# Kernel tuning notes

Hardware: AMD Instinct MI355X
Metric: run time of the kernel (lower is better)

## Reference

```python
import jax, jax.numpy as jnp
import numpy as np

N_NODES = 100000
IN_FEATURES = 128
OUT_FEATURES = 128
N_EDGES = 3200000


def setup_inputs() -> dict:
    key = jax.random.key(0)
    k1, k2, k3, k4, k5 = jax.random.split(key, 5)
    node_features = jax.random.normal(k1, (N_NODES, IN_FEATURES), dtype=jnp.float32)
    edge_index = jax.random.randint(k2, (2, N_EDGES), 0, N_NODES, dtype=jnp.int64)
    edge_values = jax.random.uniform(k3, (N_EDGES,), dtype=jnp.float32)
    # Linear layer params (PyTorch nn.Linear: y = x @ W.T + b)
    bound = 1.0 / np.sqrt(IN_FEATURES)
    W = jax.random.uniform(k4, (OUT_FEATURES, IN_FEATURES), minval=-bound, maxval=bound, dtype=jnp.float32)
    b = jax.random.uniform(k5, (OUT_FEATURES,), minval=-bound, maxval=bound, dtype=jnp.float32)
    return {"node_features": node_features, "edge_index": edge_index,
            "edge_values": edge_values, "W": W, "b": b}


def reference(node_features, edge_index, edge_values, W, b):
    n_nodes = node_features.shape[0]
    row, col = edge_index[0], edge_index[1]
    # zero diagonal entries, then square edge values
    vals = jnp.where(row != col, edge_values, jnp.zeros_like(edge_values)) ** 2
    # linear transform: [N, F_out]
    wx = node_features @ W.T + b
    # SpMM: temp[i] = sum_e vals[e] * wx[col[e]] for row[e] == i
    messages = vals[:, None] * wx[col]          # [E, F_out] gather + scale
    temp = jax.ops.segment_sum(messages, row, num_segments=n_nodes)  # scatter-add
    # Hadamard product
    return wx * temp
```

## Files before the change

kernel.cpp:

```cpp
#include <hip/hip_runtime.h>
#include <hip/hip_bf16.h>

#define F 128
#define RB 196
#define NB_MAX 511
#define BIN_CAP 16
#define NBLK_BIN 512
#define NXS 16

typedef __attribute__((ext_vector_type(8))) short bf16x8;
typedef __attribute__((ext_vector_type(4))) float f32x4;

static __device__ __forceinline__ short f2bf(float f) {
    __hip_bfloat16 h = __float2bfloat16(f);
    return __builtin_bit_cast(short, h);
}

__global__ __launch_bounds__(256) void gemm_mfma_kernel(
    const float* __restrict__ X, const float* __restrict__ W,
    const float* __restrict__ bias, float* __restrict__ wxf,
    __hip_bfloat16* __restrict__ wxh, int nrows)
{
    __shared__ short xs[128][136];
    __shared__ short wt[128][136];
    __shared__ float bsh[128];

    int t = threadIdx.x;
    long row0 = (long)blockIdx.x * 128;

    {
        int r = t >> 1, h = t & 1;
        const float4* src = reinterpret_cast<const float4*>(W + r * F + h * 64);
#pragma unroll
        for (int i = 0; i < 16; ++i) {
            float4 v = src[i];
            short4 s;
            s.x = f2bf(v.x); s.y = f2bf(v.y); s.z = f2bf(v.z); s.w = f2bf(v.w);
            *reinterpret_cast<short4*>(&wt[r][h * 64 + i * 4]) = s;
        }
        if (t < 128) bsh[t] = bias[t];
    }
    {
        int r = t >> 1, h = t & 1;
        long gr = row0 + r; if (gr > nrows - 1) gr = nrows - 1;
        const float4* src = reinterpret_cast<const float4*>(X + gr * F + h * 64);
#pragma unroll
        for (int i = 0; i < 16; ++i) {
            float4 v = src[i];
            short4 s;
            s.x = f2bf(v.x); s.y = f2bf(v.y); s.z = f2bf(v.z); s.w = f2bf(v.w);
            *reinterpret_cast<short4*>(&xs[r][h * 64 + i * 4]) = s;
        }
    }
    __syncthreads();

    int wave = t >> 6, lane = t & 63;
    int l15 = lane & 15, lg = lane >> 4;
    int mrow = wave * 32;

    float bj[8];
#pragma unroll
    for (int nf = 0; nf < 8; ++nf) bj[nf] = bsh[nf * 16 + l15];

    f32x4 acc[2][8] = {};

#pragma unroll
    for (int ks = 0; ks < 4; ++ks) {
        bf16x8 a0 = *reinterpret_cast<const bf16x8*>(&xs[mrow + l15][ks * 32 + lg * 8]);
        bf16x8 a1 = *reinterpret_cast<const bf16x8*>(&xs[mrow + 16 + l15][ks * 32 + lg * 8]);
#pragma unroll
        for (int nf = 0; nf < 8; ++nf) {
            bf16x8 bfr = *reinterpret_cast<const bf16x8*>(&wt[nf * 16 + l15][ks * 32 + lg * 8]);
            acc[0][nf] = __builtin_amdgcn_mfma_f32_16x16x32_bf16(a0, bfr, acc[0][nf], 0, 0, 0);
            acc[1][nf] = __builtin_amdgcn_mfma_f32_16x16x32_bf16(a1, bfr, acc[1][nf], 0, 0, 0);
        }
    }

#pragma unroll
    for (int mf = 0; mf < 2; ++mf) {
#pragma unroll
        for (int i = 0; i < 4; ++i) {
            long grow = row0 + mrow + mf * 16 + lg * 4 + i;
            if (grow < nrows) {
#pragma unroll
                for (int nf = 0; nf < 8; ++nf) {
                    float v = acc[mf][nf][i] + bj[nf];
                    int col = nf * 16 + l15;
                    wxf[grow * F + col] = v;
                    wxh[grow * F + col] = __float2bfloat16(v);
                }
            }
        }
    }
}

__global__ __launch_bounds__(256) void bin_edges_kernel(
    const int* __restrict__ rowi, const int* __restrict__ coli,
    const float* __restrict__ ev, int* __restrict__ cur2,
    int2* __restrict__ arena1, int E, int NB, int CAPX)
{
    __shared__ int2 bins[NB_MAX][BIN_CAP];
    __shared__ int  cnt[NB_MAX];
    __shared__ int  flushed[NB_MAX];

    int t = threadIdx.x;
    int x = blockIdx.x & (NXS - 1);
    for (int i = t; i < NB; i += 256) { cnt[i] = 0; flushed[i] = 0; }
    __syncthreads();

    long per   = ((long)E + NBLK_BIN - 1) / NBLK_BIN;
    long start = (long)blockIdx.x * per;
    long endE  = start + per; if (endE > E) endE = E;

    int r = 0, c = 0; float v = 0.f;
    {
        long i0 = start + t;
        if (i0 < endE) { r = rowi[i0]; c = coli[i0]; v = ev[i0]; }
    }

    for (long base = start; base < endE; base += 256) {
        if (base + t < endE) {
            float v2 = (r != c) ? v * v : 0.0f;
            int b  = r / RB;
            int rl = r - b * RB;
            int pos = atomicAdd(&cnt[b], 1);
            bins[b][pos & (BIN_CAP - 1)] = make_int2((rl << 17) | c, __float_as_int(v2));
        }
        int rn = 0, cn = 0; float vn = 0.f;
        {
            long i2 = base + 256 + t;
            if (i2 < endE) { rn = rowi[i2]; cn = coli[i2]; vn = ev[i2]; }
        }
        __syncthreads();
        for (int bb = t; bb < NB; bb += 256) {
            while (cnt[bb] - flushed[bb] >= 8) {
                int gpos = atomicAdd(&cur2[x * NB + bb], 8);
                if (gpos + 8 <= CAPX) {
                    const int2* src = &bins[bb][flushed[bb] & (BIN_CAP - 1)];
                    int2* dst = &arena1[((size_t)x * NB + bb) * CAPX + gpos];
                    const int4* s4 = (const int4*)src;
                    int4* d4 = (int4*)dst;
                    d4[0] = s4[0]; d4[1] = s4[1]; d4[2] = s4[2]; d4[3] = s4[3];
                }
                flushed[bb] += 8;
            }
        }
        __syncthreads();
        r = rn; c = cn; v = vn;
    }
    for (int bb = t; bb < NB; bb += 256) {
        int rem = cnt[bb] - flushed[bb];
        if (rem > 0) {
            int gpos = atomicAdd(&cur2[x * NB + bb], rem);
            if (gpos + rem <= CAPX) {
                int2* dst = &arena1[((size_t)x * NB + bb) * CAPX + gpos];
                for (int k = 0; k < rem; ++k)
                    dst[k] = bins[bb][(flushed[bb] + k) & (BIN_CAP - 1)];
            }
        }
    }
}

__global__ __launch_bounds__(256) void sort_bucket_kernel(
    const int* __restrict__ cur2, const int2* __restrict__ arena1,
    int2* __restrict__ arena2, int2* __restrict__ rowoff,
    int nrows, int NB, int CAPX, int CAP)
{
    __shared__ int rcnt[RB];
    __shared__ int rcur[RB];
    __shared__ int sscan[256];

    int b = blockIdx.x;
    int t = threadIdx.x;
    int2* dst = arena2 + (size_t)b * CAP;

    for (int i = t; i < RB; i += 256) rcnt[i] = 0;
    __syncthreads();

    for (int x = 0; x < NXS; ++x) {
        int n_x = cur2[x * NB + b]; if (n_x > CAPX) n_x = CAPX;
        const int2* seg = arena1 + ((size_t)x * NB + b) * CAPX;
        for (int i = t; i < n_x; i += 256)
            atomicAdd(&rcnt[seg[i].x >> 17], 1);
    }
    __syncthreads();

    int v = (t < RB) ? rcnt[t] : 0;
    sscan[t] = v;
    __syncthreads();
#pragma unroll
    for (int d = 1; d < 256; d <<= 1) {
        int u = (t >= d) ? sscan[t - d] : 0;
        __syncthreads();
        sscan[t] += u;
        __syncthreads();
    }
    if (t < RB) {
        int start = sscan[t] - v;
        rcur[t] = start;
        int grow = b * RB + t;
        if (grow < nrows)
            rowoff[grow] = make_int2(b * CAP + start, b * CAP + start + v);
    }
    __syncthreads();

    for (int x = 0; x < NXS; ++x) {
        int n_x = cur2[x * NB + b]; if (n_x > CAPX) n_x = CAPX;
        const int2* seg = arena1 + ((size_t)x * NB + b) * CAPX;
        for (int i = t; i < n_x; i += 256) {
            int2 rec = seg[i];
            int pos = atomicAdd(&rcur[rec.x >> 17], 1);
            if (pos < CAP) dst[pos] = rec;
        }
    }
}

__global__ __launch_bounds__(256) void agg_row_kernel(
    const int2* __restrict__ rowoff, const int2* __restrict__ arena2,
    const unsigned int* __restrict__ wxh32, float* __restrict__ outwx,
    int nrows)
{
    int wid  = (blockIdx.x * 256 + threadIdx.x) >> 6;
    int lane = threadIdx.x & 63;
    if (wid >= nrows) return;

    int2 se   = rowoff[wid];
    int start = __builtin_amdgcn_readfirstlane(se.x);
    int end   = __builtin_amdgcn_readfirstlane(se.y);

    float accx = 0.f, accy = 0.f;
    int e = start;
    for (; e + 3 < end; e += 4) {
        int2 r0 = arena2[e];
        int2 r1 = arena2[e + 1];
        int2 r2 = arena2[e + 2];
        int2 r3 = arena2[e + 3];
        unsigned int g0 = wxh32[(size_t)(r0.x & 0x1FFFF) * 64 + lane];
        unsigned int g1 = wxh32[(size_t)(r1.x & 0x1FFFF) * 64 + lane];
        unsigned int g2 = wxh32[(size_t)(r2.x & 0x1FFFF) * 64 + lane];
        unsigned int g3 = wxh32[(size_t)(r3.x & 0x1FFFF) * 64 + lane];
        float v0 = __int_as_float(r0.y), v1 = __int_as_float(r1.y);
        float v2 = __int_as_float(r2.y), v3 = __int_as_float(r3.y);
        accx = fmaf(v0, __uint_as_float(g0 << 16), accx);
        accy = fmaf(v0, __uint_as_float(g0 & 0xFFFF0000u), accy);
        accx = fmaf(v1, __uint_as_float(g1 << 16), accx);
        accy = fmaf(v1, __uint_as_float(g1 & 0xFFFF0000u), accy);
        accx = fmaf(v2, __uint_as_float(g2 << 16), accx);
        accy = fmaf(v2, __uint_as_float(g2 & 0xFFFF0000u), accy);
        accx = fmaf(v3, __uint_as_float(g3 << 16), accx);
        accy = fmaf(v3, __uint_as_float(g3 & 0xFFFF0000u), accy);
    }
    for (; e < end; ++e) {
        int2 r0 = arena2[e];
        unsigned int g0 = wxh32[(size_t)(r0.x & 0x1FFFF) * 64 + lane];
        float v0 = __int_as_float(r0.y);
        accx = fmaf(v0, __uint_as_float(g0 << 16), accx);
        accy = fmaf(v0, __uint_as_float(g0 & 0xFFFF0000u), accy);
    }

    float2 wr = *reinterpret_cast<const float2*>(outwx + (size_t)wid * F + lane * 2);
    float2 o;
    o.x = wr.x * accx;
    o.y = wr.y * accy;
    *reinterpret_cast<float2*>(outwx + (size_t)wid * F + lane * 2) = o;
}

__global__ __launch_bounds__(256) void edge_scatter_kernel(
    const int* __restrict__ rowi, const int* __restrict__ coli,
    const float* __restrict__ ev, const float* __restrict__ wx,
    float* __restrict__ temp, int E)
{
    int tid = blockIdx.x * 256 + threadIdx.x;
    int e   = tid >> 5;
    if (e >= E) return;
    int lane = tid & 31;
    int r = rowi[e];
    int c = coli[e];
    if (r == c) return;
    float v = ev[e];
    v = v * v;
    const float4 wv = *reinterpret_cast<const float4*>(wx + (size_t)c * F + lane * 4);
    float* tp = temp + (size_t)r * F + lane * 4;
    atomicAdd(tp + 0, v * wv.x);
    atomicAdd(tp + 1, v * wv.y);
    atomicAdd(tp + 2, v * wv.z);
    atomicAdd(tp + 3, v * wv.w);
}

__global__ __launch_bounds__(256) void finalize_kernel(
    float* __restrict__ out, const float* __restrict__ temp, int n4)
{
    int i = blockIdx.x * 256 + threadIdx.x;
    if (i >= n4) return;
    float4 o  = reinterpret_cast<float4*>(out)[i];
    float4 tv = reinterpret_cast<const float4*>(temp)[i];
    o.x *= tv.x; o.y *= tv.y; o.z *= tv.z; o.w *= tv.w;
    reinterpret_cast<float4*>(out)[i] = o;
}

__global__ void Interaction_GraphConvolution_55963423867450_kernel() {}

extern "C" void kernel_launch(void* const* d_in, const int* in_sizes, int n_in,
                              void* d_out, int out_size, void* d_ws, size_t ws_size,
                              hipStream_t stream)
{
    const float* X  = (const float*)d_in[0];
    const int*   ei = (const int*)d_in[1];
    const float* ev = (const float*)d_in[2];
    const float* W  = (const float*)d_in[3];
    const float* b  = (const float*)d_in[4];
    float* out = (float*)d_out;

    int nrows = in_sizes[0] / F;
    int E     = in_sizes[2];
    const int* rowi = ei;
    const int* coli = ei + E;

    int gblocks = (int)((nrows + 127) / 128);

    int NB = (nrows + RB - 1) / RB;
    if (NB <= NB_MAX) {
        long avg = (long)E / NB;
        int CAP  = (int)(((avg * 9) / 8 + 192 + 7) & ~7L);
        int CAPX = (int)(((avg / NXS) * 5 / 4 + 64 + 7) & ~7L);

        char* p = (char*)d_ws;
        __hip_bfloat16* wxh = (__hip_bfloat16*)p;
        p += (size_t)nrows * F * sizeof(__hip_bfloat16);
        int* cur2 = (int*)p;
        p += (size_t)NXS * NB * sizeof(int);
        p = (char*)(((uintptr_t)p + 63) & ~(uintptr_t)63);
        int2* rowoff = (int2*)p;
        p += (size_t)nrows * sizeof(int2);
        int2* arena1 = (int2*)p;
        p += (size_t)NXS * NB * CAPX * sizeof(int2);
        int2* arena2 = (int2*)p;
        p += (size_t)NB * CAP * sizeof(int2);
        size_t need = (size_t)(p - (char*)d_ws);

        if (ws_size >= need) {
            hipMemsetAsync(cur2, 0, (size_t)NXS * NB * sizeof(int), stream);
            gemm_mfma_kernel<<<gblocks, 256, 0, stream>>>(X, W, b, out, wxh, nrows);
            bin_edges_kernel<<<NBLK_BIN, 256, 0, stream>>>(rowi, coli, ev, cur2,
                                                           arena1, E, NB, CAPX);
            sort_bucket_kernel<<<NB, 256, 0, stream>>>(cur2, arena1, arena2,
                                                       rowoff, nrows, NB, CAPX, CAP);
            int ablocks = (int)(((long)nrows * 64 + 255) / 256);
            agg_row_kernel<<<ablocks, 256, 0, stream>>>(rowoff, arena2,
                                                        (const unsigned int*)wxh,
                                                        out, nrows);
            return;
        }
    }

    float* temp = (float*)d_ws;
    hipMemsetAsync(temp, 0, (size_t)nrows * F * sizeof(float), stream);
    __hip_bfloat16* wxh_dummy = (__hip_bfloat16*)((char*)d_ws + (size_t)nrows * F * sizeof(float));
    gemm_mfma_kernel<<<(int)((nrows + 127) / 128), 256, 0, stream>>>(X, W, b, out, wxh_dummy, nrows);
    long ethreads = (long)E * 32;
    int  eblocks32 = (int)((ethreads + 255) / 256);
    edge_scatter_kernel<<<eblocks32, 256, 0, stream>>>(rowi, coli, ev, out, temp, E);
    int n4 = nrows * F / 4;
    finalize_kernel<<<(n4 + 255) / 256, 256, 0, stream>>>(out, temp, n4);
}
```

Measured before the change: 224.6 us.

## Pack edge records into 32-bit bf16-value/col words and sort by column group

```diff
diff --git a/kernel.cpp b/kernel.cpp
--- a/kernel.cpp
+++ b/kernel.cpp
@@ -7,10 +7,16 @@
 #define BIN_CAP 16
 #define NBLK_BIN 512
 #define NXS 16
+#define NCG 16
+#define KEYS (RB * NCG)
 
 typedef __attribute__((ext_vector_type(8))) short bf16x8;
 typedef __attribute__((ext_vector_type(4))) float f32x4;
 
+static __device__ __forceinline__ unsigned short f2bfbits(float f) {
+    __hip_bfloat16 h = __float2bfloat16(f);
+    return __builtin_bit_cast(unsigned short, h);
+}
 static __device__ __forceinline__ short f2bf(float f) {
     __hip_bfloat16 h = __float2bfloat16(f);
     return __builtin_bit_cast(short, h);
@@ -163,30 +169,35 @@
 
 __global__ __launch_bounds__(256) void sort_bucket_kernel(
     const int* __restrict__ cur2, const int2* __restrict__ arena1,
-    int2* __restrict__ arena2, int2* __restrict__ rowoff,
+    unsigned int* __restrict__ arena2, int2* __restrict__ rowoff,
     int nrows, int NB, int CAPX, int CAP)
 {
-    __shared__ int rcnt[RB];
-    __shared__ int rcur[RB];
+    __shared__ int koff[KEYS];
     __shared__ int sscan[256];
 
     int b = blockIdx.x;
     int t = threadIdx.x;
-    int2* dst = arena2 + (size_t)b * CAP;
-
-    for (int i = t; i < RB; i += 256) rcnt[i] = 0;
+    unsigned int* dst = arena2 + (size_t)b * CAP;
+
+    for (int i = t; i < KEYS; i += 256) koff[i] = 0;
     __syncthreads();
 
     for (int x = 0; x < NXS; ++x) {
         int n_x = cur2[x * NB + b]; if (n_x > CAPX) n_x = CAPX;
         const int2* seg = arena1 + ((size_t)x * NB + b) * CAPX;
-        for (int i = t; i < n_x; i += 256)
-            atomicAdd(&rcnt[seg[i].x >> 17], 1);
-    }
-    __syncthreads();
-
-    int v = (t < RB) ? rcnt[t] : 0;
-    sscan[t] = v;
+        for (int i = t; i < n_x; i += 256) {
+            int rx = seg[i].x;
+            int key = (rx >> 17) * NCG + ((rx & 0x1FFFF) >> 13);
+            atomicAdd(&koff[key], 1);
+        }
+    }
+    __syncthreads();
+
+    const int PER = (KEYS + 255) / 256;
+    int lo = t * PER, hi = lo + PER; if (hi > KEYS) hi = KEYS; if (lo > KEYS) lo = KEYS;
+    int s = 0;
+    for (int i = lo; i < hi; ++i) s += koff[i];
+    sscan[t] = s;
     __syncthreads();
 #pragma unroll
     for (int d = 1; d < 256; d <<= 1) {
@@ -195,12 +206,22 @@
         sscan[t] += u;
         __syncthreads();
     }
+    int total = sscan[255];
+    int run = (t == 0) ? 0 : sscan[t - 1];
+    for (int i = lo; i < hi; ++i) {
+        int c0 = koff[i];
+        koff[i] = run;
+        run += c0;
+    }
+    __syncthreads();
+
     if (t < RB) {
-        int start = sscan[t] - v;
-        rcur[t] = start;
         int grow = b * RB + t;
-        if (grow < nrows)
-            rowoff[grow] = make_int2(b * CAP + start, b * CAP + start + v);
+        if (grow < nrows) {
+            int start = koff[t * NCG];
+            int end   = (t == RB - 1) ? total : koff[(t + 1) * NCG];
+            rowoff[grow] = make_int2(b * CAP + start, b * CAP + end);
+        }
     }
     __syncthreads();
 
@@ -209,14 +230,18 @@
         const int2* seg = arena1 + ((size_t)x * NB + b) * CAPX;
         for (int i = t; i < n_x; i += 256) {
             int2 rec = seg[i];
-            int pos = atomicAdd(&rcur[rec.x >> 17], 1);
-            if (pos < CAP) dst[pos] = rec;
+            int c = rec.x & 0x1FFFF;
+            int key = (rec.x >> 17) * NCG + (c >> 13);
+            int pos = atomicAdd(&koff[key], 1);
+            unsigned int pk = ((unsigned int)f2bfbits(__int_as_float(rec.y)) << 17)
+                              | (unsigned int)c;
+            if (pos < CAP) dst[pos] = pk;
         }
     }
 }
 
 __global__ __launch_bounds__(256) void agg_row_kernel(
-    const int2* __restrict__ rowoff, const int2* __restrict__ arena2,
+    const int2* __restrict__ rowoff, const unsigned int* __restrict__ arena2,
     const unsigned int* __restrict__ wxh32, float* __restrict__ outwx,
     int nrows)
 {
@@ -231,16 +256,18 @@
     float accx = 0.f, accy = 0.f;
     int e = start;
     for (; e + 3 < end; e += 4) {
-        int2 r0 = arena2[e];
-        int2 r1 = arena2[e + 1];
-        int2 r2 = arena2[e + 2];
-        int2 r3 = arena2[e + 3];
-        unsigned int g0 = wxh32[(size_t)(r0.x & 0x1FFFF) * 64 + lane];
-        unsigned int g1 = wxh32[(size_t)(r1.x & 0x1FFFF) * 64 + lane];
-        unsigned int g2 = wxh32[(size_t)(r2.x & 0x1FFFF) * 64 + lane];
-        unsigned int g3 = wxh32[(size_t)(r3.x & 0x1FFFF) * 64 + lane];
-        float v0 = __int_as_float(r0.y), v1 = __int_as_float(r1.y);
-        float v2 = __int_as_float(r2.y), v3 = __int_as_float(r3.y);
+        unsigned int p0 = arena2[e];
+        unsigned int p1 = arena2[e + 1];
+        unsigned int p2 = arena2[e + 2];
+        unsigned int p3 = arena2[e + 3];
+        unsigned int g0 = wxh32[(size_t)(p0 & 0x1FFFF) * 64 + lane];
+        unsigned int g1 = wxh32[(size_t)(p1 & 0x1FFFF) * 64 + lane];
+        unsigned int g2 = wxh32[(size_t)(p2 & 0x1FFFF) * 64 + lane];
+        unsigned int g3 = wxh32[(size_t)(p3 & 0x1FFFF) * 64 + lane];
+        float v0 = __uint_as_float((p0 >> 17) << 16);
+        float v1 = __uint_as_float((p1 >> 17) << 16);
+        float v2 = __uint_as_float((p2 >> 17) << 16);
+        float v3 = __uint_as_float((p3 >> 17) << 16);
         accx = fmaf(v0, __uint_as_float(g0 << 16), accx);
         accy = fmaf(v0, __uint_as_float(g0 & 0xFFFF0000u), accy);
         accx = fmaf(v1, __uint_as_float(g1 << 16), accx);
@@ -251,9 +278,9 @@
         accy = fmaf(v3, __uint_as_float(g3 & 0xFFFF0000u), accy);
     }
     for (; e < end; ++e) {
-        int2 r0 = arena2[e];
-        unsigned int g0 = wxh32[(size_t)(r0.x & 0x1FFFF) * 64 + lane];
-        float v0 = __int_as_float(r0.y);
+        unsigned int p0 = arena2[e];
+        unsigned int g0 = wxh32[(size_t)(p0 & 0x1FFFF) * 64 + lane];
+        float v0 = __uint_as_float((p0 >> 17) << 16);
         accx = fmaf(v0, __uint_as_float(g0 << 16), accx);
         accy = fmaf(v0, __uint_as_float(g0 & 0xFFFF0000u), accy);
     }
@@ -319,7 +346,7 @@
     int gblocks = (int)((nrows + 127) / 128);
 
     int NB = (nrows + RB - 1) / RB;
-    if (NB <= NB_MAX) {
+    if (NB <= NB_MAX && nrows < (1 << 17)) {
         long avg = (long)E / NB;
         int CAP  = (int)(((avg * 9) / 8 + 192 + 7) & ~7L);
         int CAPX = (int)(((avg / NXS) * 5 / 4 + 64 + 7) & ~7L);
@@ -334,8 +361,8 @@
         p += (size_t)nrows * sizeof(int2);
         int2* arena1 = (int2*)p;
         p += (size_t)NXS * NB * CAPX * sizeof(int2);
-        int2* arena2 = (int2*)p;
-        p += (size_t)NB * CAP * sizeof(int2);
+        unsigned int* arena2 = (unsigned int*)p;
+        p += (size_t)NB * CAP * sizeof(unsigned int);
         size_t need = (size_t)(p - (char*)d_ws);
 
         if (ws_size >= need) {
```

New measurement: 218.9 us. -2.6%, faster.
